# Optimization experiments

Measured on AMD Instinct MI355X. Metric: run time of the kernel, lower is better.

Reference implementation:

```python
import jax, jax.numpy as jnp
import numpy as np

N_USERS = 100000
N_ITEMS = 50000
N_NODES = N_USERS + N_ITEMS
EMB_DIM = 64
N_EDGES = 4000000
N_LAYERS = 3
BATCH = 4096


def setup_inputs() -> dict:
    key = jax.random.key(0)
    k = jax.random.split(key, 7)
    return {
        "user_emb": jax.random.normal(k[0], (N_USERS, EMB_DIM), dtype=jnp.float32) * 0.1,
        "item_emb": jax.random.normal(k[1], (N_ITEMS, EMB_DIM), dtype=jnp.float32) * 0.1,
        "vals": jax.random.uniform(k[2], (N_EDGES,), dtype=jnp.float32),
        "src": jax.random.randint(k[3], (N_EDGES,), 0, N_NODES, dtype=jnp.int32),
        "dst": jax.random.randint(k[4], (N_EDGES,), 0, N_NODES, dtype=jnp.int32),
        "users": jax.random.randint(k[5], (BATCH,), 0, N_USERS, dtype=jnp.int32),
        "items": jax.random.randint(k[6], (BATCH,), 0, N_ITEMS, dtype=jnp.int32),
    }


def _propagate(user_emb, item_emb, vals, src, dst):
    # all_emb: [N, D]; sparse adjacency A given as COO (src -> dst, weight vals)
    all_emb = jnp.concatenate([user_emb, item_emb], axis=0)
    acc = all_emb  # running sum over layers (layer 0 included)
    emb = all_emb
    for _ in range(N_LAYERS):
        # SpMM: out[d] = sum_{e: dst[e]==d} vals[e] * emb[src[e]]
        msgs = vals[:, None] * emb[src]               # [E, D]
        emb = jax.ops.segment_sum(msgs, dst, num_segments=N_NODES)
        acc = acc + emb
    light_out = acc / jnp.float32(N_LAYERS + 1)       # mean over stacked layers
    return light_out[:N_USERS], light_out[N_USERS:]


def reference(user_emb, item_emb, vals, src, dst, users, items):
    all_users, all_items = _propagate(user_emb, item_emb, vals, src, dst)
    u = all_users[users]                              # [B, D]
    i = all_items[items]                              # [B, D]
    gamma = jnp.sum(u * i, axis=1)                    # [B]
    return gamma
```

## Files before the change

kernel.cpp:

```cpp
#include <hip/hip_runtime.h>
#include <hip/hip_bf16.h>

#define N_USERS 100000
#define N_ITEMS 50000
#define N_NODES 150000
#define DIM 64
#define N_EDGES 4000000
#define BATCH 4096

#define NBKT 512
#define BW 294
#define STRIDE 9216
#define PA_EDGES 4096
#define PA_ITER 16
#define PA_BLOCKS ((N_EDGES + PA_EDGES - 1) / PA_EDGES)
#define CVT_BLOCKS (N_NODES * DIM / 4 / 256)
#define BS_ITER 16

__device__ __forceinline__ float blo(unsigned int u) { return __uint_as_float(u << 16); }
__device__ __forceinline__ float bhi(unsigned int u) { return __uint_as_float(u & 0xffff0000u); }
__device__ __forceinline__ unsigned int f2b(float f) {
    unsigned int x = __float_as_uint(f);
    return (x + 0x7fffu + ((x >> 16) & 1u)) >> 16;
}
__device__ __forceinline__ unsigned int pack2(float a, float b) {
    return f2b(a) | (f2b(b) << 16);
}

typedef float v2f __attribute__((ext_vector_type(2)));

__global__ void __launch_bounds__(256, 4) k_cvtpart(
        const float* __restrict__ uemb, const float* __restrict__ iemb,
        ushort* __restrict__ ebf0,
        const int* __restrict__ src, const int* __restrict__ dst,
        const float* __restrict__ vals,
        int* __restrict__ gcur, int2* __restrict__ tmp) {
    __shared__ int cnt[NBKT];
    __shared__ int base_s[NBKT];
    __shared__ int off_s[NBKT];
    __shared__ int2 rec_s[PA_EDGES];
    __shared__ ushort bin_s[PA_EDGES];
    int t = threadIdx.x;
    if (blockIdx.x >= PA_BLOCKS) {
        int tid = (blockIdx.x - PA_BLOCKS) * 256 + t;
        int i = tid * 4;
        if (i >= N_NODES * DIM) return;
        const float* srcp = (i < N_USERS * DIM) ? (uemb + i) : (iemb + (i - N_USERS * DIM));
        float4 v;
        v.x = __builtin_nontemporal_load(srcp + 0);
        v.y = __builtin_nontemporal_load(srcp + 1);
        v.z = __builtin_nontemporal_load(srcp + 2);
        v.w = __builtin_nontemporal_load(srcp + 3);
        *(uint2*)(ebf0 + i) = make_uint2(pack2(v.x, v.y), pack2(v.z, v.w));
        return;
    }
    int myb[PA_ITER];
    int mykey[PA_ITER];
    int myval[PA_ITER];
    size_t base = (size_t)blockIdx.x * PA_EDGES;
#pragma unroll
    for (int it = 0; it < PA_ITER; it++) {
        size_t i = base + (size_t)it * 256 + t;
        if (i < N_EDGES) {
            myb[it] = __builtin_nontemporal_load(dst + i);
            mykey[it] = __builtin_nontemporal_load(src + i);
            myval[it] = __float_as_int(__builtin_nontemporal_load(vals + i));
        } else {
            myb[it] = -1;
        }
    }
    for (int i = t; i < NBKT; i += 256) cnt[i] = 0;
    __syncthreads();
#pragma unroll
    for (int it = 0; it < PA_ITER; it++) {
        int d = myb[it];
        if (d >= 0) {
            int b = d / BW;
            mykey[it] = (mykey[it] << 9) | (d - b * BW);
            myb[it] = b;
            atomicAdd(&cnt[b], 1);
        }
    }
    __syncthreads();
    for (int i = t; i < NBKT; i += 256) {
        int c = cnt[i];
        base_s[i] = (c > 0) ? atomicAdd(&gcur[i], c) : 0;
    }
    if (t < 64) {
        int lane = t;
        int carry = 0;
        for (int c = 0; c < NBKT / 64; c++) {
            int i = c * 64 + lane;
            int x = cnt[i];
            int incl = x;
            for (int o = 1; o < 64; o <<= 1) {
                int y = __shfl_up(incl, o);
                if (lane >= o) incl += y;
            }
            off_s[i] = carry + incl - x;
            carry += __shfl(incl, 63);
        }
    }
    __syncthreads();
    for (int i = t; i < NBKT; i += 256) cnt[i] = 0;
    __syncthreads();
#pragma unroll
    for (int it = 0; it < PA_ITER; it++) {
        int b = myb[it];
        if (b >= 0) {
            int pos = off_s[b] + atomicAdd(&cnt[b], 1);
            rec_s[pos] = make_int2(mykey[it], myval[it]);
            bin_s[pos] = (ushort)b;
        }
    }
    __syncthreads();
    int nrec = off_s[NBKT - 1] + cnt[NBKT - 1];
    for (int i = t; i < nrec; i += 256) {
        int2 r = rec_s[i];
        int b = bin_s[i];
        tmp[(size_t)b * STRIDE + base_s[b] + (i - off_s[b])] = r;
    }
}

__global__ void k_bsort(const int2* __restrict__ tmp, const int* __restrict__ gcur,
                        int* __restrict__ row_ptr, int2* __restrict__ fin) {
    __shared__ int cnt[BW + 64];
    __shared__ int off[BW + 64];
    __shared__ int gbase_s;
    int b = blockIdx.x, t = threadIdx.x;
    int node0 = b * BW;
    int nodes = min(BW, N_NODES - node0);
    int count = gcur[b];
    const int2* tb = tmp + (size_t)b * STRIDE;
    int2 myrec[BS_ITER];
#pragma unroll
    for (int it = 0; it < BS_ITER; it++) {
        int e = it * 512 + t;
        myrec[it] = (e < count) ? tb[e] : make_int2(-1, 0);
    }
    if (t < 64) {
        int ssum = 0;
#pragma unroll
        for (int j = 0; j < 8; j++) {
            int idx = t * 8 + j;
            if (idx < b) ssum += gcur[idx];
        }
        for (int o = 32; o; o >>= 1) ssum += __shfl_xor(ssum, o);
        if (t == 0) gbase_s = ssum;
    }
    for (int i = t; i < BW + 64; i += 512) cnt[i] = 0;
    __syncthreads();
    int gbase = gbase_s;
#pragma unroll
    for (int it = 0; it < BS_ITER; it++)
        if (myrec[it].x >= 0) atomicAdd(&cnt[myrec[it].x & 511], 1);
    for (int e = BS_ITER * 512 + t; e < count; e += 512)
        atomicAdd(&cnt[tb[e].x & 511], 1);
    __syncthreads();
    if (t < 64) {
        int lane = t;
        int carry = 0;
        for (int c = 0; c < 5; c++) {
            int i = c * 64 + lane;
            int x = (i < nodes) ? cnt[i] : 0;
            int incl = x;
            for (int o = 1; o < 64; o <<= 1) {
                int y = __shfl_up(incl, o);
                if (lane >= o) incl += y;
            }
            if (i <= nodes) off[i] = carry + incl - x;
            carry += __shfl(incl, 63);
        }
    }
    __syncthreads();
    for (int i = t; i <= nodes; i += 512)
        if (node0 + i <= N_NODES) row_ptr[node0 + i] = gbase + off[i];
    __syncthreads();
#pragma unroll
    for (int it = 0; it < BS_ITER; it++) {
        int2 r = myrec[it];
        if (r.x >= 0) {
            int pos = gbase + atomicAdd(&off[r.x & 511], 1);
            fin[pos] = make_int2(r.x >> 9, r.y);
        }
    }
    for (int e = BS_ITER * 512 + t; e < count; e += 512) {
        int2 r = tb[e];
        int pos = gbase + atomicAdd(&off[r.x & 511], 1);
        fin[pos] = make_int2(r.x >> 9, r.y);
    }
}


#define EDGE_FMA(r, u, A0, A1, A2, A3)                                        \
    {                                                                         \
        float vf = __int_as_float((r).y);                                     \
        v2f vv = {vf, vf};                                                    \
        v2f f0 = {blo((u).x), bhi((u).x)};                                    \
        v2f f1 = {blo((u).y), bhi((u).y)};                                    \
        v2f f2 = {blo((u).z), bhi((u).z)};                                    \
        v2f f3 = {blo((u).w), bhi((u).w)};                                    \
        A0 = __builtin_elementwise_fma(vv, f0, A0);                           \
        A1 = __builtin_elementwise_fma(vv, f1, A1);                           \
        A2 = __builtin_elementwise_fma(vv, f2, A2);                           \
        A3 = __builtin_elementwise_fma(vv, f3, A3);                           \
    }

#define GATHER16(basec, r) (*(const uint4*)((basec) + ((((unsigned int)(r).x) << 7) | qoff)))
#define REC8(basec, i) (*(const int2*)((basec) + (((unsigned int)(i)) << 3)))

#define BURST32(basec)                                                        \
    {                                                                         \
        int e1 = e + 8, e2 = e + 16, e3 = e + 24;                             \
        int2 ra = REC8(basec, e);                                             \
        int2 rb = REC8(basec, min(e1, last));                                 \
        int2 rc = REC8(basec, min(e2, last));                                 \
        int2 rd = REC8(basec, min(e3, last));                                 \
        rb.y = (e1 < end) ? rb.y : 0;                                         \
        rc.y = (e2 < end) ? rc.y : 0;                                         \
        rd.y = (e3 < end) ? rd.y : 0;                                         \
        uint4 ua = GATHER16(einc, ra);                                        \
        uint4 ub = GATHER16(einc, rb);                                        \
        uint4 uc = GATHER16(einc, rc);                                        \
        uint4 ud = GATHER16(einc, rd);                                        \
        EDGE_FMA(ra, ua, A0, A1, A2, A3);                                     \
        EDGE_FMA(rb, ub, A0, A1, A2, A3);                                     \
        EDGE_FMA(rc, uc, A0, A1, A2, A3);                                     \
        EDGE_FMA(rd, ud, A0, A1, A2, A3);                                     \
        e += 32;                                                              \
    }

__global__ void k_spmm16(const ushort* __restrict__ ein, ushort* __restrict__ eout,
                         const int* __restrict__ row_ptr, const int2* __restrict__ fin) {
    int wave = (blockIdx.x * blockDim.x + threadIdx.x) >> 6;
    if (wave >= N_NODES) return;
    int lane = threadIdx.x & 63;
    int g = lane >> 3;
    int q = lane & 7;
    unsigned int qoff = (unsigned int)q << 4;
    const char* einc = (const char*)ein;
    const char* finc = (const char*)fin;
    int start = row_ptr[wave], end = row_ptr[wave + 1];
    int last = max(start, end - 1);
    v2f A0 = {0.f, 0.f}, A1 = {0.f, 0.f}, A2 = {0.f, 0.f}, A3 = {0.f, 0.f};
    int e = start + g;
    while (e < end) BURST32(finc);
#pragma unroll
    for (int off = 8; off < 64; off <<= 1) {
        A0.x += __shfl_xor(A0.x, off);
        A0.y += __shfl_xor(A0.y, off);
        A1.x += __shfl_xor(A1.x, off);
        A1.y += __shfl_xor(A1.y, off);
        A2.x += __shfl_xor(A2.x, off);
        A2.y += __shfl_xor(A2.y, off);
        A3.x += __shfl_xor(A3.x, off);
        A3.y += __shfl_xor(A3.y, off);
    }
    if (lane < 8) {
        uint4 p;
        p.x = pack2(A0.x, A0.y);
        p.y = pack2(A1.x, A1.y);
        p.z = pack2(A2.x, A2.y);
        p.w = pack2(A3.x, A3.y);
        *(uint4*)(eout + (size_t)wave * DIM + q * 8) = p;
    }
}

__global__ void k_samp(const ushort* __restrict__ ein, const int* __restrict__ row_ptr,
                       const int2* __restrict__ fin, const int* __restrict__ users,
                       const int* __restrict__ items, float* __restrict__ l3) {
    int slot = (blockIdx.x * blockDim.x + threadIdx.x) >> 6;
    if (slot >= 2 * BATCH) return;
    int lane = threadIdx.x & 63;
    int g = lane >> 3;
    int q = lane & 7;
    unsigned int qoff = (unsigned int)q << 4;
    const char* einc = (const char*)ein;
    const char* finc = (const char*)fin;
    int node = (slot < BATCH) ? users[slot] : (items[slot - BATCH] + N_USERS);
    int start = row_ptr[node], end = row_ptr[node + 1];
    int last = max(start, end - 1);
    v2f A0 = {0.f, 0.f}, A1 = {0.f, 0.f}, A2 = {0.f, 0.f}, A3 = {0.f, 0.f};
    int e = start + g;
    while (e < end) BURST32(finc);
#pragma unroll
    for (int off = 8; off < 64; off <<= 1) {
        A0.x += __shfl_xor(A0.x, off);
        A0.y += __shfl_xor(A0.y, off);
        A1.x += __shfl_xor(A1.x, off);
        A1.y += __shfl_xor(A1.y, off);
        A2.x += __shfl_xor(A2.x, off);
        A2.y += __shfl_xor(A2.y, off);
        A3.x += __shfl_xor(A3.x, off);
        A3.y += __shfl_xor(A3.y, off);
    }
    if (lane < 8) {
        float* row = l3 + (size_t)slot * DIM + q * 8;
        *(float4*)row = make_float4(A0.x, A0.y, A1.x, A1.y);
        *(float4*)(row + 4) = make_float4(A2.x, A2.y, A3.x, A3.y);
    }
}

__global__ void k_gacc0(const float* __restrict__ uemb, const float* __restrict__ iemb,
                        const ushort* __restrict__ emb, const int* __restrict__ users,
                        const int* __restrict__ items, float* __restrict__ accU,
                        float* __restrict__ accI) {
    int i = blockIdx.x * blockDim.x + threadIdx.x;
    if (i >= 2 * BATCH * DIM) return;
    int j = (i < BATCH * DIM) ? i : i - BATCH * DIM;
    int b = j >> 6, l = j & 63;
    if (i < BATCH * DIM) {
        int n = users[b];
        unsigned int u = emb[(size_t)n * DIM + l];
        accU[j] = uemb[(size_t)n * DIM + l] + __uint_as_float(u << 16);
    } else {
        int n = items[b];
        unsigned int u = emb[(size_t)(n + N_USERS) * DIM + l];
        accI[j] = iemb[(size_t)n * DIM + l] + __uint_as_float(u << 16);
    }
}

__global__ void k_gacc(const ushort* __restrict__ emb, const int* __restrict__ users,
                       const int* __restrict__ items, float* __restrict__ accU,
                       float* __restrict__ accI) {
    int i = blockIdx.x * blockDim.x + threadIdx.x;
    if (i >= 2 * BATCH * DIM) return;
    int j = (i < BATCH * DIM) ? i : i - BATCH * DIM;
    int b = j >> 6, l = j & 63;
    if (i < BATCH * DIM) {
        unsigned int u = emb[(size_t)users[b] * DIM + l];
        accU[j] += __uint_as_float(u << 16);
    } else {
        unsigned int u = emb[(size_t)(items[b] + N_USERS) * DIM + l];
        accI[j] += __uint_as_float(u << 16);
    }
}

__global__ void k_dot(const float* __restrict__ accU, const float* __restrict__ accI,
                      const float* __restrict__ l3, float* __restrict__ out) {
    int b = (blockIdx.x * blockDim.x + threadIdx.x) >> 6;
    if (b >= BATCH) return;
    int lane = threadIdx.x & 63;
    float aU = accU[b * 64 + lane] + l3[(size_t)b * 64 + lane];
    float aI = accI[b * 64 + lane] + l3[(size_t)(BATCH + b) * 64 + lane];
    float p = aU * aI;
    for (int off = 32; off; off >>= 1) p += __shfl_xor(p, off);
    if (lane == 0) out[b] = p * (1.0f / 16.0f);
}


extern "C" void kernel_launch(void* const* d_in, const int* in_sizes, int n_in,
                              void* d_out, int out_size, void* d_ws, size_t ws_size,
                              hipStream_t stream) {
    const float* user_emb = (const float*)d_in[0];
    const float* item_emb = (const float*)d_in[1];
    const float* vals = (const float*)d_in[2];
    const int* src = (const int*)d_in[3];
    const int* dst = (const int*)d_in[4];
    const int* users = (const int*)d_in[5];
    const int* items = (const int*)d_in[6];
    float* out = (float*)d_out;

    char* ws = (char*)d_ws;
    size_t off = 0;
    auto alloc = [&](size_t bytes) {
        char* p = ws + off;
        off += (bytes + 255) & ~(size_t)255;
        return p;
    };
    ushort* ebf0 = (ushort*)alloc((size_t)N_NODES * DIM * 2);
    ushort* ebf1 = (ushort*)alloc((size_t)N_NODES * DIM * 2);
    ushort* ebf2 = (ushort*)alloc((size_t)N_NODES * DIM * 2);
    int2* fin = (int2*)alloc((size_t)N_EDGES * 8);
    int* row_ptr = (int*)alloc((size_t)(N_NODES + 1) * 4);
    int* gcur = (int*)alloc((size_t)NBKT * 4);
    float* l3 = (float*)alloc((size_t)2 * BATCH * DIM * 4);
    float* accU = (float*)alloc((size_t)BATCH * DIM * 4);
    float* accI = (float*)alloc((size_t)BATCH * DIM * 4);
    int2* tmp = (int2*)ebf1;

    hipMemsetAsync(gcur, 0, (size_t)NBKT * 4, stream);

    k_cvtpart<<<PA_BLOCKS + CVT_BLOCKS, 256, 0, stream>>>(
        user_emb, item_emb, ebf0, src, dst, vals, gcur, tmp);
    k_bsort<<<NBKT, 512, 0, stream>>>(tmp, gcur, row_ptr, fin);

    int gb = (2 * BATCH * DIM + 255) / 256;
    int spmm_blocks = (N_NODES * 64 + 255) / 256;
    k_spmm16<<<spmm_blocks, 256, 0, stream>>>(ebf0, ebf1, row_ptr, fin);
    k_gacc0<<<gb, 256, 0, stream>>>(user_emb, item_emb, ebf1, users, items, accU, accI);
    k_spmm16<<<spmm_blocks, 256, 0, stream>>>(ebf1, ebf2, row_ptr, fin);
    k_gacc<<<gb, 256, 0, stream>>>(ebf2, users, items, accU, accI);
    k_samp<<<(2 * BATCH * 64 + 255) / 256, 256, 0, stream>>>(ebf2, row_ptr, fin, users, items, l3);

    k_dot<<<(BATCH * 64 + 255) / 256, 256, 0, stream>>>(accU, accI, l3, out);
}
```

Measured before the change: 327.2 us.

## Fuse sampled third layer, accumulation and dot; stage bucket sort in LDS

The separate gather-accumulate kernels, the sampled third-layer SpMM and the dot kernel are merged into one kernel. For each batch pair it computes both sampled rows, adds layers 0–2 read directly from the embedding buffers, and reduces the dot product. This removes three launches and the intermediate accU/accI/l3 buffers. Separately, the bucket sort now scatters records into a dynamic shared-memory buffer (72KB) and writes them out contiguously, replacing scattered global stores. The large LDS allocation may lower occupancy of the sort kernel.

```diff
diff --git a/kernel.cpp b/kernel.cpp
--- a/kernel.cpp
+++ b/kernel.cpp
@@ -127,6 +127,7 @@
     __shared__ int cnt[BW + 64];
     __shared__ int off[BW + 64];
     __shared__ int gbase_s;
+    extern __shared__ int2 rec2[];
     int b = blockIdx.x, t = threadIdx.x;
     int node0 = b * BW;
     int nodes = min(BW, N_NODES - node0);
@@ -180,15 +181,17 @@
     for (int it = 0; it < BS_ITER; it++) {
         int2 r = myrec[it];
         if (r.x >= 0) {
-            int pos = gbase + atomicAdd(&off[r.x & 511], 1);
-            fin[pos] = make_int2(r.x >> 9, r.y);
+            int pos = atomicAdd(&off[r.x & 511], 1);
+            rec2[pos] = make_int2(r.x >> 9, r.y);
         }
     }
     for (int e = BS_ITER * 512 + t; e < count; e += 512) {
         int2 r = tb[e];
-        int pos = gbase + atomicAdd(&off[r.x & 511], 1);
-        fin[pos] = make_int2(r.x >> 9, r.y);
-    }
+        int pos = atomicAdd(&off[r.x & 511], 1);
+        rec2[pos] = make_int2(r.x >> 9, r.y);
+    }
+    __syncthreads();
+    for (int i = t; i < count; i += 512) fin[gbase + i] = rec2[i];
 }
 
 
@@ -209,25 +212,25 @@
 #define GATHER16(basec, r) (*(const uint4*)((basec) + ((((unsigned int)(r).x) << 7) | qoff)))
 #define REC8(basec, i) (*(const int2*)((basec) + (((unsigned int)(i)) << 3)))
 
-#define BURST32(basec)                                                        \
+#define BURST32(basec, e, end, last, X0, X1, X2, X3)                          \
     {                                                                         \
-        int e1 = e + 8, e2 = e + 16, e3 = e + 24;                             \
-        int2 ra = REC8(basec, e);                                             \
+        int e1 = (e) + 8, e2 = (e) + 16, e3 = (e) + 24;                       \
+        int2 ra = REC8(basec, (e));                                           \
         int2 rb = REC8(basec, min(e1, last));                                 \
         int2 rc = REC8(basec, min(e2, last));                                 \
         int2 rd = REC8(basec, min(e3, last));                                 \
-        rb.y = (e1 < end) ? rb.y : 0;                                         \
-        rc.y = (e2 < end) ? rc.y : 0;                                         \
-        rd.y = (e3 < end) ? rd.y : 0;                                         \
+        rb.y = (e1 < (end)) ? rb.y : 0;                                       \
+        rc.y = (e2 < (end)) ? rc.y : 0;                                       \
+        rd.y = (e3 < (end)) ? rd.y : 0;                                       \
         uint4 ua = GATHER16(einc, ra);                                        \
         uint4 ub = GATHER16(einc, rb);                                        \
         uint4 uc = GATHER16(einc, rc);                                        \
         uint4 ud = GATHER16(einc, rd);                                        \
-        EDGE_FMA(ra, ua, A0, A1, A2, A3);                                     \
-        EDGE_FMA(rb, ub, A0, A1, A2, A3);                                     \
-        EDGE_FMA(rc, uc, A0, A1, A2, A3);                                     \
-        EDGE_FMA(rd, ud, A0, A1, A2, A3);                                     \
-        e += 32;                                                              \
+        EDGE_FMA(ra, ua, X0, X1, X2, X3);                                     \
+        EDGE_FMA(rb, ub, X0, X1, X2, X3);                                     \
+        EDGE_FMA(rc, uc, X0, X1, X2, X3);                                     \
+        EDGE_FMA(rd, ud, X0, X1, X2, X3);                                     \
+        (e) += 32;                                                            \
     }
 
 __global__ void k_spmm16(const ushort* __restrict__ ein, ushort* __restrict__ eout,
@@ -244,7 +247,7 @@
     int last = max(start, end - 1);
     v2f A0 = {0.f, 0.f}, A1 = {0.f, 0.f}, A2 = {0.f, 0.f}, A3 = {0.f, 0.f};
     int e = start + g;
-    while (e < end) BURST32(finc);
+    while (e < end) BURST32(finc, e, end, last, A0, A1, A2, A3);
 #pragma unroll
     for (int off = 8; off < 64; off <<= 1) {
         A0.x += __shfl_xor(A0.x, off);
@@ -266,23 +269,36 @@
     }
 }
 
-__global__ void k_samp(const ushort* __restrict__ ein, const int* __restrict__ row_ptr,
-                       const int2* __restrict__ fin, const int* __restrict__ users,
-                       const int* __restrict__ items, float* __restrict__ l3) {
-    int slot = (blockIdx.x * blockDim.x + threadIdx.x) >> 6;
-    if (slot >= 2 * BATCH) return;
+__global__ void k_sampdot(const float* __restrict__ uemb, const float* __restrict__ iemb,
+                          const ushort* __restrict__ ebf1, const ushort* __restrict__ ebf2,
+                          const int* __restrict__ row_ptr, const int2* __restrict__ fin,
+                          const int* __restrict__ users, const int* __restrict__ items,
+                          float* __restrict__ out) {
+    int b = (blockIdx.x * blockDim.x + threadIdx.x) >> 6;
+    if (b >= BATCH) return;
     int lane = threadIdx.x & 63;
     int g = lane >> 3;
     int q = lane & 7;
     unsigned int qoff = (unsigned int)q << 4;
-    const char* einc = (const char*)ein;
+    const char* einc = (const char*)ebf2;
     const char* finc = (const char*)fin;
-    int node = (slot < BATCH) ? users[slot] : (items[slot - BATCH] + N_USERS);
-    int start = row_ptr[node], end = row_ptr[node + 1];
-    int last = max(start, end - 1);
+    int iu = users[b];
+    int ii = items[b];
+    int nu = iu, ni = ii + N_USERS;
     v2f A0 = {0.f, 0.f}, A1 = {0.f, 0.f}, A2 = {0.f, 0.f}, A3 = {0.f, 0.f};
-    int e = start + g;
-    while (e < end) BURST32(finc);
+    {
+        int start = row_ptr[nu], end = row_ptr[nu + 1];
+        int last = max(start, end - 1);
+        int e = start + g;
+        while (e < end) BURST32(finc, e, end, last, A0, A1, A2, A3);
+    }
+    v2f B0 = {0.f, 0.f}, B1 = {0.f, 0.f}, B2 = {0.f, 0.f}, B3 = {0.f, 0.f};
+    {
+        int start = row_ptr[ni], end = row_ptr[ni + 1];
+        int last = max(start, end - 1);
+        int e = start + g;
+        while (e < end) BURST32(finc, e, end, last, B0, B1, B2, B3);
+    }
 #pragma unroll
     for (int off = 8; off < 64; off <<= 1) {
         A0.x += __shfl_xor(A0.x, off);
@@ -293,58 +309,40 @@
         A2.y += __shfl_xor(A2.y, off);
         A3.x += __shfl_xor(A3.x, off);
         A3.y += __shfl_xor(A3.y, off);
-    }
-    if (lane < 8) {
-        float* row = l3 + (size_t)slot * DIM + q * 8;
-        *(float4*)row = make_float4(A0.x, A0.y, A1.x, A1.y);
-        *(float4*)(row + 4) = make_float4(A2.x, A2.y, A3.x, A3.y);
-    }
-}
-
-__global__ void k_gacc0(const float* __restrict__ uemb, const float* __restrict__ iemb,
-                        const ushort* __restrict__ emb, const int* __restrict__ users,
-                        const int* __restrict__ items, float* __restrict__ accU,
-                        float* __restrict__ accI) {
-    int i = blockIdx.x * blockDim.x + threadIdx.x;
-    if (i >= 2 * BATCH * DIM) return;
-    int j = (i < BATCH * DIM) ? i : i - BATCH * DIM;
-    int b = j >> 6, l = j & 63;
-    if (i < BATCH * DIM) {
-        int n = users[b];
-        unsigned int u = emb[(size_t)n * DIM + l];
-        accU[j] = uemb[(size_t)n * DIM + l] + __uint_as_float(u << 16);
-    } else {
-        int n = items[b];
-        unsigned int u = emb[(size_t)(n + N_USERS) * DIM + l];
-        accI[j] = iemb[(size_t)n * DIM + l] + __uint_as_float(u << 16);
-    }
-}
-
-__global__ void k_gacc(const ushort* __restrict__ emb, const int* __restrict__ users,
-                       const int* __restrict__ items, float* __restrict__ accU,
-                       float* __restrict__ accI) {
-    int i = blockIdx.x * blockDim.x + threadIdx.x;
-    if (i >= 2 * BATCH * DIM) return;
-    int j = (i < BATCH * DIM) ? i : i - BATCH * DIM;
-    int b = j >> 6, l = j & 63;
-    if (i < BATCH * DIM) {
-        unsigned int u = emb[(size_t)users[b] * DIM + l];
-        accU[j] += __uint_as_float(u << 16);
-    } else {
-        unsigned int u = emb[(size_t)(items[b] + N_USERS) * DIM + l];
-        accI[j] += __uint_as_float(u << 16);
-    }
-}
-
-__global__ void k_dot(const float* __restrict__ accU, const float* __restrict__ accI,
-                      const float* __restrict__ l3, float* __restrict__ out) {
-    int b = (blockIdx.x * blockDim.x + threadIdx.x) >> 6;
-    if (b >= BATCH) return;
-    int lane = threadIdx.x & 63;
-    float aU = accU[b * 64 + lane] + l3[(size_t)b * 64 + lane];
-    float aI = accI[b * 64 + lane] + l3[(size_t)(BATCH + b) * 64 + lane];
-    float p = aU * aI;
-    for (int off = 32; off; off >>= 1) p += __shfl_xor(p, off);
+        B0.x += __shfl_xor(B0.x, off);
+        B0.y += __shfl_xor(B0.y, off);
+        B1.x += __shfl_xor(B1.x, off);
+        B1.y += __shfl_xor(B1.y, off);
+        B2.x += __shfl_xor(B2.x, off);
+        B2.y += __shfl_xor(B2.y, off);
+        B3.x += __shfl_xor(B3.x, off);
+        B3.y += __shfl_xor(B3.y, off);
+    }
+    {
+        const float4* fp = (const float4*)(uemb + (size_t)nu * DIM + q * 8);
+        float4 fa = fp[0], fb = fp[1];
+        uint4 u1 = *(const uint4*)(ebf1 + (size_t)nu * DIM + q * 8);
+        uint4 u2 = *(const uint4*)(ebf2 + (size_t)nu * DIM + q * 8);
+        A0.x += fa.x + blo(u1.x) + blo(u2.x); A0.y += fa.y + bhi(u1.x) + bhi(u2.x);
+        A1.x += fa.z + blo(u1.y) + blo(u2.y); A1.y += fa.w + bhi(u1.y) + bhi(u2.y);
+        A2.x += fb.x + blo(u1.z) + blo(u2.z); A2.y += fb.y + bhi(u1.z) + bhi(u2.z);
+        A3.x += fb.z + blo(u1.w) + blo(u2.w); A3.y += fb.w + bhi(u1.w) + bhi(u2.w);
+    }
+    {
+        const float4* fp = (const float4*)(iemb + (size_t)ii * DIM + q * 8);
+        float4 fa = fp[0], fb = fp[1];
+        uint4 u1 = *(const uint4*)(ebf1 + (size_t)ni * DIM + q * 8);
+        uint4 u2 = *(const uint4*)(ebf2 + (size_t)ni * DIM + q * 8);
+        B0.x += fa.x + blo(u1.x) + blo(u2.x); B0.y += fa.y + bhi(u1.x) + bhi(u2.x);
+        B1.x += fa.z + blo(u1.y) + blo(u2.y); B1.y += fa.w + bhi(u1.y) + bhi(u2.y);
+        B2.x += fb.x + blo(u1.z) + blo(u2.z); B2.y += fb.y + bhi(u1.z) + bhi(u2.z);
+        B3.x += fb.z + blo(u1.w) + blo(u2.w); B3.y += fb.w + bhi(u1.w) + bhi(u2.w);
+    }
+    float p = A0.x * B0.x + A0.y * B0.y + A1.x * B1.x + A1.y * B1.y +
+              A2.x * B2.x + A2.y * B2.y + A3.x * B3.x + A3.y * B3.y;
+    p += __shfl_xor(p, 1);
+    p += __shfl_xor(p, 2);
+    p += __shfl_xor(p, 4);
     if (lane == 0) out[b] = p * (1.0f / 16.0f);
 }
 
@@ -374,24 +372,17 @@
     int2* fin = (int2*)alloc((size_t)N_EDGES * 8);
     int* row_ptr = (int*)alloc((size_t)(N_NODES + 1) * 4);
     int* gcur = (int*)alloc((size_t)NBKT * 4);
-    float* l3 = (float*)alloc((size_t)2 * BATCH * DIM * 4);
-    float* accU = (float*)alloc((size_t)BATCH * DIM * 4);
-    float* accI = (float*)alloc((size_t)BATCH * DIM * 4);
     int2* tmp = (int2*)ebf1;
 
     hipMemsetAsync(gcur, 0, (size_t)NBKT * 4, stream);
 
     k_cvtpart<<<PA_BLOCKS + CVT_BLOCKS, 256, 0, stream>>>(
         user_emb, item_emb, ebf0, src, dst, vals, gcur, tmp);
-    k_bsort<<<NBKT, 512, 0, stream>>>(tmp, gcur, row_ptr, fin);
-
-    int gb = (2 * BATCH * DIM + 255) / 256;
+    k_bsort<<<NBKT, 512, (size_t)STRIDE * 8, stream>>>(tmp, gcur, row_ptr, fin);
+
     int spmm_blocks = (N_NODES * 64 + 255) / 256;
     k_spmm16<<<spmm_blocks, 256, 0, stream>>>(ebf0, ebf1, row_ptr, fin);
-    k_gacc0<<<gb, 256, 0, stream>>>(user_emb, item_emb, ebf1, users, items, accU, accI);
     k_spmm16<<<spmm_blocks, 256, 0, stream>>>(ebf1, ebf2, row_ptr, fin);
-    k_gacc<<<gb, 256, 0, stream>>>(ebf2, users, items, accU, accI);
-    k_samp<<<(2 * BATCH * 64 + 255) / 256, 256, 0, stream>>>(ebf2, row_ptr, fin, users, items, l3);
-
-    k_dot<<<(BATCH * 64 + 255) / 256, 256, 0, stream>>>(accU, accI, l3, out);
-}
+    k_sampdot<<<(BATCH * 64 + 255) / 256, 256, 0, stream>>>(
+        user_emb, item_emb, ebf1, ebf2, row_ptr, fin, users, items, out);
+}
```

Measured after the change: 310.6 us. 1.05x faster.
